# Optimization experiments

Hardware: AMD Instinct MI355X
Metric: run time of the kernel (lower is better)

Reference implementation:

```python
import jax, jax.numpy as jnp
import numpy as np
from itertools import combinations_with_replacement

MAX_DEGREE = 4
INPUT_DIM = 16
BATCH = 32768

# Static gather-index tables: one [n_terms_d, d] int array per degree d.
IDX = {d: np.asarray(list(combinations_with_replacement(range(INPUT_DIM), d)), dtype=np.int32)
       for d in range(1, MAX_DEGREE + 1)}
P = 1 + sum(IDX[d].shape[0] for d in IDX)  # total polynomial features (4845)


def setup_inputs() -> dict:
    key = jax.random.key(0)
    k1, k2 = jax.random.split(key)
    x = jax.random.normal(k1, (BATCH, INPUT_DIM), dtype=jnp.float32)
    W = jax.random.normal(k2, (1, P), dtype=jnp.float32) * 0.02
    b = jnp.zeros((1,), dtype=jnp.float32)
    M_raw = jnp.zeros((), dtype=jnp.float32)
    return {"x": x, "W": W, "b": b, "M_raw": M_raw}


def _transform(x, M_raw):
    # M = sigmoid(M_raw) * (max_degree - 1) + 1  (soft degree threshold)
    M = jax.nn.sigmoid(M_raw) * (MAX_DEGREE - 1) + 1.0
    feats = [jnp.ones((x.shape[0], 1), dtype=x.dtype)]  # bias/constant term
    for d in range(1, MAX_DEGREE + 1):
        w = jax.nn.sigmoid(10.0 * (M - d + 0.5))  # per-degree soft weight
        idx = IDX[d]  # [n_d, d]
        prod = x[:, idx[:, 0]]  # [B, n_d]
        for j in range(1, d):  # small fixed loop over degree, not data dims
            prod = prod * x[:, idx[:, j]]
        feats.append(prod * w)
    return jnp.concatenate(feats, axis=1)  # [B, P]


def reference(x, W, b, M_raw):
    xt = _transform(x, M_raw)               # [B, P]
    logits = xt @ W.T + b                   # [B, 1]
    return jax.nn.sigmoid(logits)
```

## Files before the change

kernel.cpp:

```cpp
#include <hip/hip_runtime.h>
#include <math.h>

#define DIMS 16
#define BATCH 32768

__device__ constexpr int cnt2(int j){ return 16 - j; }
__device__ constexpr int cnt3(int j){ return (16 - j) * (17 - j) / 2; }
__device__ constexpr int cnt4(int j){ return (16 - j) * (17 - j) * (18 - j) / 6; }
__device__ constexpr int off2(int i0){ int s = 0; for (int j = 0; j < i0; ++j) s += cnt2(j); return s; }
__device__ constexpr int off3(int i0){ int s = 0; for (int j = 0; j < i0; ++j) s += cnt3(j); return s; }
__device__ constexpr int off4(int i0){ int s = 0; for (int j = 0; j < i0; ++j) s += cnt4(j); return s; }

template<int I0>
__device__ __forceinline__ void do_i0(const float* __restrict__ W,
                                      const float* __restrict__ xv,
                                      float& a1, float& a2, float& a3, float& a4)
{
    const float x0 = xv[I0];
    a1 = fmaf(W[1 + I0], x0, a1);
    int k2 = 17  + off2(I0);
    int k3 = 153 + off3(I0);
    int k4 = 969 + off4(I0);
    #pragma unroll
    for (int i1 = I0; i1 < DIMS; ++i1) {
        const float p2 = x0 * xv[i1];
        a2 = fmaf(W[k2++], p2, a2);
        #pragma unroll
        for (int i2 = i1; i2 < DIMS; ++i2) {
            const float p3 = p2 * xv[i2];
            a3 = fmaf(W[k3++], p3, a3);
            float s4 = 0.0f;
            #pragma unroll
            for (int i3 = i2; i3 < DIMS; ++i3)
                s4 = fmaf(W[k4++], xv[i3], s4);
            a4 = fmaf(p3, s4, a4);
        }
    }
}

template<int... Is>
__device__ __forceinline__ float role_partial(const float* __restrict__ W,
                                              const float* __restrict__ xv,
                                              float w1, float w2, float w3, float w4)
{
    float a1 = 0.f, a2 = 0.f, a3 = 0.f, a4 = 0.f;
    (do_i0<Is>(W, xv, a1, a2, a3, a4), ...);
    return fmaf(w1, a1, fmaf(w2, a2, fmaf(w3, a3, w4 * a4)));
}

__global__ __launch_bounds__(256, 2)
void poly_logreg_kernel(const float* __restrict__ x,
                        const float* __restrict__ W,
                        const float* __restrict__ b,
                        const float* __restrict__ M_raw,
                        float* __restrict__ out)
{
    const int lane = threadIdx.x & 63;
    const int wave = threadIdx.x >> 6;
    const int s    = (blockIdx.x << 6) + lane;

    const float M  = 3.0f / (1.0f + __expf(-M_raw[0])) + 1.0f;
    const float w1 = 1.0f / (1.0f + __expf(-10.0f * (M - 1.0f + 0.5f)));
    const float w2 = 1.0f / (1.0f + __expf(-10.0f * (M - 2.0f + 0.5f)));
    const float w3 = 1.0f / (1.0f + __expf(-10.0f * (M - 3.0f + 0.5f)));
    const float w4 = 1.0f / (1.0f + __expf(-10.0f * (M - 4.0f + 0.5f)));

    float xv[DIMS];
    const float4* xp = reinterpret_cast<const float4*>(x + (size_t)s * DIMS);
    #pragma unroll
    for (int q = 0; q < 4; ++q) {
        const float4 v = xp[q];
        xv[q * 4 + 0] = v.x; xv[q * 4 + 1] = v.y;
        xv[q * 4 + 2] = v.z; xv[q * 4 + 3] = v.w;
    }

    float partial;
    if (wave == 0)      partial = role_partial<0, 6>(W, xv, w1, w2, w3, w4);
    else if (wave == 1) partial = role_partial<1, 5, 13, 14, 15>(W, xv, w1, w2, w3, w4);
    else if (wave == 2) partial = role_partial<2, 4, 11, 12>(W, xv, w1, w2, w3, w4);
    else                partial = role_partial<3, 7, 8, 9, 10>(W, xv, w1, w2, w3, w4);

    __shared__ float part_lds[3][64];
    if (wave > 0) part_lds[wave - 1][lane] = partial;
    __syncthreads();

    if (wave == 0) {
        const float logit = W[0] + b[0] + partial
                          + part_lds[0][lane] + part_lds[1][lane] + part_lds[2][lane];
        out[s] = 1.0f / (1.0f + __expf(-logit));
    }
}

extern "C" void kernel_launch(void* const* d_in, const int* in_sizes, int n_in,
                              void* d_out, int out_size, void* d_ws, size_t ws_size,
                              hipStream_t stream)
{
    const float* x     = (const float*)d_in[0];
    const float* W     = (const float*)d_in[1];
    const float* b     = (const float*)d_in[2];
    const float* M_raw = (const float*)d_in[3];
    float* out = (float*)d_out;

    const int blocks = BATCH / 64;
    poly_logreg_kernel<<<blocks, 256, 0, stream>>>(x, W, b, M_raw, out);
}
```

Before: 13.29 us.

## Recast polynomial logistic regression as bf16 MFMA quadratic form over pair features

```diff
diff --git a/kernel.cpp b/kernel.cpp
--- a/kernel.cpp
+++ b/kernel.cpp
@@ -1,93 +1,213 @@
 #include <hip/hip_runtime.h>
 #include <math.h>
-
-#define DIMS 16
+#include <utility>
+
+#define DIMS  16
 #define BATCH 32768
-
-__device__ constexpr int cnt2(int j){ return 16 - j; }
-__device__ constexpr int cnt3(int j){ return (16 - j) * (17 - j) / 2; }
-__device__ constexpr int cnt4(int j){ return (16 - j) * (17 - j) * (18 - j) / 6; }
-__device__ constexpr int off2(int i0){ int s = 0; for (int j = 0; j < i0; ++j) s += cnt2(j); return s; }
-__device__ constexpr int off3(int i0){ int s = 0; for (int j = 0; j < i0; ++j) s += cnt3(j); return s; }
-__device__ constexpr int off4(int i0){ int s = 0; for (int j = 0; j < i0; ++j) s += cnt4(j); return s; }
-
-template<int I0>
-__device__ __forceinline__ void do_i0(const float* __restrict__ W,
-                                      const float* __restrict__ xv,
-                                      float& a1, float& a2, float& a3, float& a4)
+#define NPAIR 136
+#define MP 160
+#define KP 160
+#define NB 128
+#define NMT 5
+#define NKK 10
+#define NNT 4
+
+typedef short  s16x8  __attribute__((ext_vector_type(8)));
+typedef float  f32x16 __attribute__((ext_vector_type(16)));
+
+#define A_ELEMS (NKK*NMT*64*8)
+#define P_ELEMS (NKK*NNT*64*8)
+#define A_BYTES (A_ELEMS*2)
+#define P_BYTES (P_ELEMS*2)
+#define RED_OFF (A_BYTES + P_BYTES)
+#define LDS_BYTES (RED_OFF + 8*32*4)
+
+constexpr int pairlex(int i0, int i1) {
+    int s = 0; for (int j = 0; j < i0; ++j) s += (DIMS - j); return s + (i1 - i0);
+}
+constexpr int cnt3(int j) { return (DIMS - j) * (DIMS + 1 - j) / 2; }
+constexpr int cnt4(int j) { return (DIMS - j) * (DIMS + 1 - j) * (DIMS + 2 - j) / 6; }
+constexpr int off3(int i0) { int s = 0; for (int j = 0; j < i0; ++j) s += cnt3(j); return s; }
+constexpr int off4(int i0) { int s = 0; for (int j = 0; j < i0; ++j) s += cnt4(j); return s; }
+constexpr int w3base(int i0) { return 1 + DIMS + NPAIR + off3(i0); }
+constexpr int w4base(int i0, int i1) {
+    int s = off4(i0); for (int b = i0; b < i1; ++b) s += cnt3(b);
+    return 1 + DIMS + NPAIR + 816 + s;
+}
+constexpr int pid_i0(int pid) {
+    int i0 = 0, rem = pid; while (rem >= DIMS - i0) { rem -= DIMS - i0; ++i0; } return i0;
+}
+constexpr int pid_i1(int pid) {
+    int i0 = 0, rem = pid; while (rem >= DIMS - i0) { rem -= DIMS - i0; ++i0; } return i0 + rem;
+}
+static_assert(pairlex(15,15) == 135 && off3(DIMS) == 816 && off4(DIMS) == 3876, "combi");
+static_assert(w4base(15,15) == 4844 && w3base(15) == 968, "wtail");
+
+struct RowMeta { short qs, qe, wb, gs; };
+struct RowTab  { RowMeta m[MP]; };
+constexpr RowTab make_rowtab() {
+    RowTab t{};
+    for (int r = 0; r < MP; ++r) {
+        RowMeta rm{0,0,0,4};
+        if (r < NPAIR) {
+            int i0 = pid_i0(r), i1 = pid_i1(r);
+            rm = RowMeta{ (short)pairlex(i1,i1), (short)NPAIR, (short)w4base(i0,i1), 0 };
+        } else if (r < NPAIR + DIMS) {
+            int i0 = r - NPAIR;
+            rm = RowMeta{ (short)pairlex(i0,i0), (short)NPAIR, (short)w3base(i0), 1 };
+        } else if (r == 152) {
+            rm = RowMeta{ 0, (short)NPAIR, 17, 2 };
+        } else if (r == 153) {
+            rm = RowMeta{ (short)NPAIR, (short)(NPAIR+DIMS), 1, 3 };
+        }
+        t.m[r] = rm;
+    }
+    return t;
+}
+__device__ __constant__ RowTab ROWTAB = make_rowtab();
+
+__device__ __forceinline__ ushort f2bf(float f) {
+    union { float f; unsigned u; } v{f};
+    return (ushort)((v.u + 0x7FFF + ((v.u >> 16) & 1)) >> 16);
+}
+__device__ __forceinline__ float bf2f(short h) {
+    union { unsigned u; float f; } v{ (unsigned)(ushort)h << 16 };
+    return v.f;
+}
+
+constexpr int p_roff(int r) {
+    return ((r >> 4) << 11) + (((r >> 2) & 1) << 8) + (r & 3) + (((r >> 3) & 1) << 2);
+}
+
+template<typename F, int... Is>
+__device__ __forceinline__ void sfor_impl(F&& f, std::integer_sequence<int, Is...>) {
+    (f(std::integral_constant<int, Is>{}), ...);
+}
+template<int N, typename F>
+__device__ __forceinline__ void sfor(F&& f) {
+    sfor_impl(static_cast<F&&>(f), std::make_integer_sequence<int, N>{});
+}
+
+template<int R>
+__device__ __forceinline__ void p_emit(ushort* __restrict__ P_sh, int sPart, const float (&xv)[DIMS]) {
+    float v;
+    if constexpr (R < NPAIR)            v = xv[pid_i0(R)] * xv[pid_i1(R)];
+    else if constexpr (R < NPAIR+DIMS)  v = xv[R - NPAIR];
+    else if constexpr (R < 154)         v = 1.0f;
+    else                                v = 0.0f;
+    P_sh[sPart + p_roff(R)] = f2bf(v);
+}
+
+template<int MT0, int NMTL>
+__device__ __forceinline__ float gemm_half(const ushort* __restrict__ A_sh,
+                                           const s16x8 (&bf)[NKK], int lane)
 {
-    const float x0 = xv[I0];
-    a1 = fmaf(W[1 + I0], x0, a1);
-    int k2 = 17  + off2(I0);
-    int k3 = 153 + off3(I0);
-    int k4 = 969 + off4(I0);
+    f32x16 acc[NMTL] = {};
     #pragma unroll
-    for (int i1 = I0; i1 < DIMS; ++i1) {
-        const float p2 = x0 * xv[i1];
-        a2 = fmaf(W[k2++], p2, a2);
+    for (int kk = 0; kk < NKK; ++kk) {
         #pragma unroll
-        for (int i2 = i1; i2 < DIMS; ++i2) {
-            const float p3 = p2 * xv[i2];
-            a3 = fmaf(W[k3++], p3, a3);
-            float s4 = 0.0f;
-            #pragma unroll
-            for (int i3 = i2; i3 < DIMS; ++i3)
-                s4 = fmaf(W[k4++], xv[i3], s4);
-            a4 = fmaf(p3, s4, a4);
-        }
-    }
-}
-
-template<int... Is>
-__device__ __forceinline__ float role_partial(const float* __restrict__ W,
-                                              const float* __restrict__ xv,
-                                              float w1, float w2, float w3, float w4)
+        for (int m = 0; m < NMTL; ++m) {
+            const s16x8 af = *reinterpret_cast<const s16x8*>(
+                A_sh + (size_t)(((kk * NMT) + MT0 + m) * 64 + lane) * 8);
+            acc[m] = __builtin_amdgcn_mfma_f32_32x32x16_bf16(af, bf[kk], acc[m], 0, 0, 0);
+        }
+    }
+    float partial = 0.0f;
+    #pragma unroll
+    for (int m = 0; m < NMTL; ++m) {
+        #pragma unroll
+        for (int reg = 0; reg < 16; ++reg) {
+            constexpr_if_dummy:;
+            const int rlo = reg & 3, rhi = reg >> 2;
+            const float mult = bf2f(bf[2 * (MT0 + m) + (rhi >> 1)][rlo + 4 * (rhi & 1)]);
+            partial = fmaf(mult, acc[m][reg], partial);
+        }
+    }
+    return partial;
+}
+
+__global__ __launch_bounds__(512, 2)
+void poly_logreg_mfma(const float* __restrict__ x,
+                      const float* __restrict__ W,
+                      const float* __restrict__ b,
+                      const float* __restrict__ M_raw,
+                      float* __restrict__ out)
 {
-    float a1 = 0.f, a2 = 0.f, a3 = 0.f, a4 = 0.f;
-    (do_i0<Is>(W, xv, a1, a2, a3, a4), ...);
-    return fmaf(w1, a1, fmaf(w2, a2, fmaf(w3, a3, w4 * a4)));
-}
-
-__global__ __launch_bounds__(256, 2)
-void poly_logreg_kernel(const float* __restrict__ x,
-                        const float* __restrict__ W,
-                        const float* __restrict__ b,
-                        const float* __restrict__ M_raw,
-                        float* __restrict__ out)
-{
-    const int lane = threadIdx.x & 63;
-    const int wave = threadIdx.x >> 6;
-    const int s    = (blockIdx.x << 6) + lane;
+    extern __shared__ char smem[];
+    ushort* A_sh = reinterpret_cast<ushort*>(smem);
+    ushort* P_sh = reinterpret_cast<ushort*>(smem + A_BYTES);
+    float*  red  = reinterpret_cast<float*>(smem + RED_OFF);
+
+    const int t    = threadIdx.x;
+    const int lane = t & 63;
+    const int wv   = t >> 6;
+
+    const int s  = t & (NB - 1);
+    const int tg = t >> 7;
+    float xv[DIMS];
+    {
+        const float4* xp = reinterpret_cast<const float4*>(
+            x + ((size_t)blockIdx.x * NB + s) * DIMS);
+        #pragma unroll
+        for (int q = 0; q < 4; ++q) {
+            const float4 v = xp[q];
+            xv[q*4+0] = v.x; xv[q*4+1] = v.y; xv[q*4+2] = v.z; xv[q*4+3] = v.w;
+        }
+    }
 
     const float M  = 3.0f / (1.0f + __expf(-M_raw[0])) + 1.0f;
-    const float w1 = 1.0f / (1.0f + __expf(-10.0f * (M - 1.0f + 0.5f)));
-    const float w2 = 1.0f / (1.0f + __expf(-10.0f * (M - 2.0f + 0.5f)));
-    const float w3 = 1.0f / (1.0f + __expf(-10.0f * (M - 3.0f + 0.5f)));
-    const float w4 = 1.0f / (1.0f + __expf(-10.0f * (M - 4.0f + 0.5f)));
-
-    float xv[DIMS];
-    const float4* xp = reinterpret_cast<const float4*>(x + (size_t)s * DIMS);
+    const float g4 = 1.0f / (1.0f + __expf(-10.0f * (M - 3.5f)));
+    const float g3 = 1.0f / (1.0f + __expf(-10.0f * (M - 2.5f)));
+    const float g2 = 1.0f / (1.0f + __expf(-10.0f * (M - 1.5f)));
+    const float g1 = 1.0f / (1.0f + __expf(-10.0f * (M - 0.5f)));
+
+    #pragma unroll 2
+    for (int i = 0; i < A_ELEMS / 512; ++i) {
+        const int id   = t + (i << 9);
+        const int e    = id & 7;
+        const int ln   = (id >> 3) & 63;
+        const int mtkk = id >> 9;
+        const int mt   = mtkk % NMT, kk = mtkk / NMT;
+        const int row  = mt * 32 + (ln & 31);
+        const int k    = kk * 16 + 4 * (ln >> 5) + (e & 3) + 8 * (e >> 2);
+        const RowMeta rm = ROWTAB.m[row];
+        float v = 0.0f;
+        if ((unsigned)(k - rm.qs) < (unsigned)(rm.qe - rm.qs)) {
+            const float g = rm.gs == 0 ? g4 : rm.gs == 1 ? g3 : rm.gs == 2 ? g2
+                          : rm.gs == 3 ? g1 : 0.0f;
+            v = g * W[rm.wb + (k - rm.qs)];
+        }
+        A_sh[id] = f2bf(v);
+    }
+
+    {
+        const int sPart = ((s >> 5) << 9) + ((s & 31) << 3);
+        switch (tg) {
+            case 0: sfor<40>([&](auto K){ p_emit<decltype(K)::value +   0>(P_sh, sPart, xv); }); break;
+            case 1: sfor<40>([&](auto K){ p_emit<decltype(K)::value +  40>(P_sh, sPart, xv); }); break;
+            case 2: sfor<40>([&](auto K){ p_emit<decltype(K)::value +  80>(P_sh, sPart, xv); }); break;
+            default:sfor<40>([&](auto K){ p_emit<decltype(K)::value + 120>(P_sh, sPart, xv); }); break;
+        }
+    }
+    __syncthreads();
+
+    const int nt = wv & 3;
+    s16x8 bf[NKK];
     #pragma unroll
-    for (int q = 0; q < 4; ++q) {
-        const float4 v = xp[q];
-        xv[q * 4 + 0] = v.x; xv[q * 4 + 1] = v.y;
-        xv[q * 4 + 2] = v.z; xv[q * 4 + 3] = v.w;
-    }
-
-    float partial;
-    if (wave == 0)      partial = role_partial<0, 6>(W, xv, w1, w2, w3, w4);
-    else if (wave == 1) partial = role_partial<1, 5, 13, 14, 15>(W, xv, w1, w2, w3, w4);
-    else if (wave == 2) partial = role_partial<2, 4, 11, 12>(W, xv, w1, w2, w3, w4);
-    else                partial = role_partial<3, 7, 8, 9, 10>(W, xv, w1, w2, w3, w4);
-
-    __shared__ float part_lds[3][64];
-    if (wave > 0) part_lds[wave - 1][lane] = partial;
+    for (int kk = 0; kk < NKK; ++kk)
+        bf[kk] = *reinterpret_cast<const s16x8*>(P_sh + (size_t)((kk * NNT + nt) * 64 + lane) * 8);
+
+    float partial = (wv >> 2) ? gemm_half<3, 2>(A_sh, bf, lane)
+                              : gemm_half<0, 3>(A_sh, bf, lane);
+    partial += __shfl_xor(partial, 32, 64);
+
+    if (lane < 32) red[wv * 32 + lane] = partial;
     __syncthreads();
 
-    if (wave == 0) {
-        const float logit = W[0] + b[0] + partial
-                          + part_lds[0][lane] + part_lds[1][lane] + part_lds[2][lane];
-        out[s] = 1.0f / (1.0f + __expf(-logit));
+    if (t < NB) {
+        const int c = t & 31, ntf = t >> 5;
+        float logit = red[ntf * 32 + c] + red[(ntf + 4) * 32 + c] + W[0] + b[0];
+        out[(size_t)blockIdx.x * NB + t] = 1.0f / (1.0f + __expf(-logit));
     }
 }
 
@@ -101,6 +221,5 @@
     const float* M_raw = (const float*)d_in[3];
     float* out = (float*)d_out;
 
-    const int blocks = BATCH / 64;
-    poly_logreg_kernel<<<blocks, 256, 0, stream>>>(x, W, b, M_raw, out);
-}
+    poly_logreg_mfma<<<BATCH / NB, 512, LDS_BYTES, stream>>>(x, W, b, M_raw, out);
+}
```

Result: slower. 37.26 us (+180.4%).

## Stage gate-scaled padded weights in LDS and factor terms by pair with balanced roles

Applied to the files above, without the earlier changes.

```diff
diff --git a/kernel.cpp b/kernel.cpp
--- a/kernel.cpp
+++ b/kernel.cpp
@@ -1,93 +1,188 @@
 #include <hip/hip_runtime.h>
 #include <math.h>
-
-#define DIMS 16
+#include <utility>
+
+#define DIMS  16
 #define BATCH 32768
-
-__device__ constexpr int cnt2(int j){ return 16 - j; }
-__device__ constexpr int cnt3(int j){ return (16 - j) * (17 - j) / 2; }
-__device__ constexpr int cnt4(int j){ return (16 - j) * (17 - j) * (18 - j) / 6; }
-__device__ constexpr int off2(int i0){ int s = 0; for (int j = 0; j < i0; ++j) s += cnt2(j); return s; }
-__device__ constexpr int off3(int i0){ int s = 0; for (int j = 0; j < i0; ++j) s += cnt3(j); return s; }
-__device__ constexpr int off4(int i0){ int s = 0; for (int j = 0; j < i0; ++j) s += cnt4(j); return s; }
-
-template<int I0>
-__device__ __forceinline__ void do_i0(const float* __restrict__ W,
-                                      const float* __restrict__ xv,
-                                      float& a1, float& a2, float& a3, float& a4)
-{
-    const float x0 = xv[I0];
-    a1 = fmaf(W[1 + I0], x0, a1);
-    int k2 = 17  + off2(I0);
-    int k3 = 153 + off3(I0);
-    int k4 = 969 + off4(I0);
-    #pragma unroll
-    for (int i1 = I0; i1 < DIMS; ++i1) {
-        const float p2 = x0 * xv[i1];
-        a2 = fmaf(W[k2++], p2, a2);
-        #pragma unroll
-        for (int i2 = i1; i2 < DIMS; ++i2) {
-            const float p3 = p2 * xv[i2];
-            a3 = fmaf(W[k3++], p3, a3);
-            float s4 = 0.0f;
-            #pragma unroll
-            for (int i3 = i2; i3 < DIMS; ++i3)
-                s4 = fmaf(W[k4++], xv[i3], s4);
-            a4 = fmaf(p3, s4, a4);
+#define NPAIR 136
+#define NROLE 4
+
+typedef float f32x4 __attribute__((ext_vector_type(4)));
+
+constexpr int pairlex(int i0, int i1){ int s=0; for(int j=0;j<i0;++j) s+=(DIMS-j); return s+(i1-i0); }
+constexpr int pid_i0(int pid){ int i0=0,rem=pid; while(rem>=DIMS-i0){rem-=DIMS-i0;++i0;} return i0; }
+constexpr int pid_i1(int pid){ int i0=0,rem=pid; while(rem>=DIMS-i0){rem-=DIMS-i0;++i0;} return i0+rem; }
+constexpr int cnt3(int j){ return (DIMS-j)*(DIMS+1-j)/2; }
+constexpr int off3(int i0){ int s=0; for(int j=0;j<i0;++j) s+=cnt3(j); return s; }
+constexpr int cnt4j(int j){ return (DIMS-j)*(DIMS+1-j)*(DIMS+2-j)/6; }
+constexpr int off4(int i0){ int s=0; for(int j=0;j<i0;++j) s+=cnt4j(j); return s; }
+constexpr int w3base(int i0,int i1){ int s=off3(i0); for(int b=i0;b<i1;++b) s+=(DIMS-b); return 1+DIMS+NPAIR+s; }
+constexpr int w4base(int i0,int i1){ int s=off4(i0); for(int b=i0;b<i1;++b) s+=cnt3(b); return 1+DIMS+NPAIR+816+s; }
+static_assert(pairlex(15,15)==135 && off3(DIMS)==816 && off4(DIMS)==3876, "combi");
+static_assert(w3base(15,15)==968 && w4base(15,15)==4844, "wtail");
+
+constexpr int align4(int n){ return (n+3)&~3; }
+constexpr int TRI(int n){ return n*(n+1)/2; }
+struct Layout { int w23[NPAIR]; int w4[NPAIR]; int w1; int total; };
+constexpr Layout make_layout(){
+    Layout L{}; int cur=0;
+    for(int p=0;p<NPAIR;++p){
+        int i1=pid_i1(p);
+        L.w23[p]=cur; cur+=align4(17-i1);
+        L.w4[p]=cur;  cur+=align4(TRI(16-i1));
+    }
+    L.w1=cur; cur+=DIMS; L.total=cur;
+    return L;
+}
+inline constexpr Layout LAY = make_layout();
+#define PADTOT 5272
+static_assert(LAY.total==PADTOT, "padtot");
+
+struct DescT { unsigned short d[PADTOT]; };
+constexpr DescT make_desc(){
+    DescT D{};
+    for(int p=0;p<NPAIR;++p){
+        int i0=pid_i0(p), i1=pid_i1(p);
+        D.d[LAY.w23[p]] = (unsigned short)((2u<<13) | (unsigned)(1+DIMS+p));
+        for(int j=0;j<DIMS-i1;++j)
+            D.d[LAY.w23[p]+1+j] = (unsigned short)((3u<<13) | (unsigned)(w3base(i0,i1)+j));
+        int k=w4base(i0,i1), idx=LAY.w4[p];
+        for(int i2=i1;i2<DIMS;++i2)
+            for(int i3=i2;i3<DIMS;++i3)
+                D.d[idx++] = (unsigned short)((4u<<13) | (unsigned)(k++));
+    }
+    for(int i=0;i<DIMS;++i) D.d[LAY.w1+i] = (unsigned short)((1u<<13) | (unsigned)(1+i));
+    return D;
+}
+__device__ __constant__ DescT DESC = make_desc();
+
+constexpr int costv(int v){ return (DIMS-v) + (DIMS+1-v)*(DIMS+2-v)/2 + 3; }
+struct Plan { int role_of[NPAIR]; int d1_role; };
+constexpr Plan make_plan(){
+    Plan p{}; long load[NROLE]={};
+    for(int v=0; v<DIMS; ++v)
+        for(int i0=0; i0<=v; ++i0){
+            int best=0;
+            for(int r=1;r<NROLE;++r) if(load[r]<load[best]) best=r;
+            p.role_of[pairlex(i0,v)]=best;
+            load[best]+=costv(v);
         }
-    }
-}
-
-template<int... Is>
-__device__ __forceinline__ float role_partial(const float* __restrict__ W,
-                                              const float* __restrict__ xv,
-                                              float w1, float w2, float w3, float w4)
-{
-    float a1 = 0.f, a2 = 0.f, a3 = 0.f, a4 = 0.f;
-    (do_i0<Is>(W, xv, a1, a2, a3, a4), ...);
-    return fmaf(w1, a1, fmaf(w2, a2, fmaf(w3, a3, w4 * a4)));
-}
-
-__global__ __launch_bounds__(256, 2)
-void poly_logreg_kernel(const float* __restrict__ x,
-                        const float* __restrict__ W,
-                        const float* __restrict__ b,
-                        const float* __restrict__ M_raw,
-                        float* __restrict__ out)
-{
-    const int lane = threadIdx.x & 63;
-    const int wave = threadIdx.x >> 6;
-    const int s    = (blockIdx.x << 6) + lane;
-
-    const float M  = 3.0f / (1.0f + __expf(-M_raw[0])) + 1.0f;
-    const float w1 = 1.0f / (1.0f + __expf(-10.0f * (M - 1.0f + 0.5f)));
-    const float w2 = 1.0f / (1.0f + __expf(-10.0f * (M - 2.0f + 0.5f)));
-    const float w3 = 1.0f / (1.0f + __expf(-10.0f * (M - 3.0f + 0.5f)));
-    const float w4 = 1.0f / (1.0f + __expf(-10.0f * (M - 4.0f + 0.5f)));
+    int best=0;
+    for(int r=1;r<NROLE;++r) if(load[r]<load[best]) best=r;
+    p.d1_role=best;
+    return p;
+}
+inline constexpr Plan PLAN = make_plan();
+
+template<typename F, int... Is>
+__device__ __forceinline__ void sfor_impl(F&& f, std::integer_sequence<int,Is...>){
+    (f(std::integral_constant<int,Is>{}), ...);
+}
+template<int N, typename F>
+__device__ __forceinline__ void sfor(F&& f){
+    sfor_impl(static_cast<F&&>(f), std::make_integer_sequence<int,N>{});
+}
+
+template<int PID>
+__device__ __forceinline__ void pair_term(const float* __restrict__ Wl,
+                                          const float (&xv)[DIMS], float& a)
+{
+    constexpr int i0=pid_i0(PID), i1=pid_i1(PID);
+    constexpr int B23=LAY.w23[PID], B4=LAY.w4[PID];
+    constexpr int N3 = DIMS-i1;
+    constexpr int NQ23 = align4(17-i1)/4;
+
+    f32x4 q23[NQ23];
+    sfor<NQ23>([&](auto C){ constexpr int c=decltype(C)::value;
+        q23[c] = *reinterpret_cast<const f32x4*>(Wl + B23 + 4*c); });
+
+    float s3 = q23[0][0];
+    sfor<N3>([&](auto J){ constexpr int j=decltype(J)::value;
+        constexpr int e = 1+j;
+        s3 = fmaf(q23[e/4][e%4], xv[i1+j], s3); });
+
+    float t = 0.f;
+    f32x4 cq{};
+    sfor<N3>([&](auto I){ constexpr int i2 = i1 + decltype(I)::value;
+        float s4 = 0.f;
+        sfor<DIMS-i2>([&](auto K){ constexpr int i3 = i2 + decltype(K)::value;
+            constexpr int e = ((DIMS-i1)+(DIMS+1-i2))*(i2-i1)/2 + (i3-i2);
+            if constexpr ((e&3)==0)
+                cq = *reinterpret_cast<const f32x4*>(Wl + B4 + e);
+            s4 = fmaf(cq[e&3], xv[i3], s4); });
+        t = fmaf(xv[i2], s4, t); });
+
+    a = fmaf(xv[i0]*xv[i1], s3 + t, a);
+}
+
+template<int R>
+__device__ __forceinline__ float role_body(const float* __restrict__ Wl,
+                                           const float (&xv)[DIMS])
+{
+    float a = 0.f;
+    sfor<NPAIR>([&](auto P){ constexpr int pid=decltype(P)::value;
+        if constexpr (PLAN.role_of[pid]==R) pair_term<pid>(Wl, xv, a); });
+    if constexpr (R==PLAN.d1_role){
+        sfor<4>([&](auto C){ constexpr int c=decltype(C)::value;
+            const f32x4 q = *reinterpret_cast<const f32x4*>(Wl + LAY.w1 + 4*c);
+            a = fmaf(q[0], xv[4*c+0], a); a = fmaf(q[1], xv[4*c+1], a);
+            a = fmaf(q[2], xv[4*c+2], a); a = fmaf(q[3], xv[4*c+3], a); });
+    }
+    return a;
+}
+
+__global__ __launch_bounds__(512, 2)
+void poly_logreg_v4(const float* __restrict__ x, const float* __restrict__ W,
+                    const float* __restrict__ b, const float* __restrict__ M_raw,
+                    float* __restrict__ out)
+{
+    __shared__ __align__(16) float Wl[PADTOT];
+    __shared__ float red[8][64];
+
+    const int t = threadIdx.x, lane = t & 63, wv = t >> 6;
+    const int role = wv & 3, grp = wv >> 2;
+    const int s = (blockIdx.x << 7) + (grp << 6) + lane;
+
+    const float4* xp = reinterpret_cast<const float4*>(x + (size_t)s * DIMS);
+    const float4 xa = xp[0], xb = xp[1], xc = xp[2], xd = xp[3];
+
+    const float M  = 3.0f/(1.0f+__expf(-M_raw[0])) + 1.0f;
+    const float g1 = 1.0f/(1.0f+__expf(-10.0f*(M-0.5f)));
+    const float g2 = 1.0f/(1.0f+__expf(-10.0f*(M-1.5f)));
+    const float g3 = 1.0f/(1.0f+__expf(-10.0f*(M-2.5f)));
+    const float g4 = 1.0f/(1.0f+__expf(-10.0f*(M-3.5f)));
+
+    for (int i = t; i < PADTOT; i += 512){
+        const unsigned short d = DESC.d[i];
+        const int deg = d >> 13, src = d & 0x1FFF;
+        const float gv = (deg==4)?g4 : (deg==3)?g3 : (deg==2)?g2 : (deg==1)?g1 : 0.0f;
+        Wl[i] = gv * W[src];
+    }
 
     float xv[DIMS];
-    const float4* xp = reinterpret_cast<const float4*>(x + (size_t)s * DIMS);
-    #pragma unroll
-    for (int q = 0; q < 4; ++q) {
-        const float4 v = xp[q];
-        xv[q * 4 + 0] = v.x; xv[q * 4 + 1] = v.y;
-        xv[q * 4 + 2] = v.z; xv[q * 4 + 3] = v.w;
-    }
-
-    float partial;
-    if (wave == 0)      partial = role_partial<0, 6>(W, xv, w1, w2, w3, w4);
-    else if (wave == 1) partial = role_partial<1, 5, 13, 14, 15>(W, xv, w1, w2, w3, w4);
-    else if (wave == 2) partial = role_partial<2, 4, 11, 12>(W, xv, w1, w2, w3, w4);
-    else                partial = role_partial<3, 7, 8, 9, 10>(W, xv, w1, w2, w3, w4);
-
-    __shared__ float part_lds[3][64];
-    if (wave > 0) part_lds[wave - 1][lane] = partial;
+    xv[0]=xa.x; xv[1]=xa.y; xv[2]=xa.z; xv[3]=xa.w;
+    xv[4]=xb.x; xv[5]=xb.y; xv[6]=xb.z; xv[7]=xb.w;
+    xv[8]=xc.x; xv[9]=xc.y; xv[10]=xc.z; xv[11]=xc.w;
+    xv[12]=xd.x; xv[13]=xd.y; xv[14]=xd.z; xv[15]=xd.w;
+
     __syncthreads();
 
-    if (wave == 0) {
-        const float logit = W[0] + b[0] + partial
-                          + part_lds[0][lane] + part_lds[1][lane] + part_lds[2][lane];
-        out[s] = 1.0f / (1.0f + __expf(-logit));
+    float a;
+    switch (role){
+        case 0:  a = role_body<0>(Wl, xv); break;
+        case 1:  a = role_body<1>(Wl, xv); break;
+        case 2:  a = role_body<2>(Wl, xv); break;
+        default: a = role_body<3>(Wl, xv); break;
+    }
+
+    red[wv][lane] = a;
+    __syncthreads();
+
+    if (t < 128){
+        const int g = t >> 6, l = t & 63;
+        const float logit = red[4*g+0][l] + red[4*g+1][l] + red[4*g+2][l] + red[4*g+3][l]
+                          + W[0] + b[0];
+        out[((size_t)blockIdx.x << 7) + t] = 1.0f/(1.0f+__expf(-logit));
     }
 }
 
@@ -101,6 +196,5 @@
     const float* M_raw = (const float*)d_in[3];
     float* out = (float*)d_out;
 
-    const int blocks = BATCH / 64;
-    poly_logreg_kernel<<<blocks, 256, 0, stream>>>(x, W, b, M_raw, out);
-}
+    poly_logreg_v4<<<BATCH/128, 512, 0, stream>>>(x, W, b, M_raw, out);
+}
```

Result: slower. 17.44 us (+31.2%).
